# Optimization experiments

Measured on AMD Instinct MI355X. Metric: run time of the kernel, lower is better.

Reference implementation:

```python
import jax, jax.numpy as jnp
import numpy as np

N = 262144   # total sentences
B = 16384    # number of bags
D = 768      # relation_dim
C = 53       # num_classes


def setup_inputs() -> dict:
    key = jax.random.key(0)
    k1, k2, k3, k4 = jax.random.split(key, 4)
    x = jax.random.normal(k1, (N, D), dtype=jnp.float32)
    # xavier_uniform-like init for the relation embedding matrix [C, D]
    limit = float(np.sqrt(6.0 / (C + D)))
    rel_weight = jax.random.uniform(k2, (C, D), dtype=jnp.float32, minval=-limit, maxval=limit)
    bias = jax.random.normal(k3, (C,), dtype=jnp.float32)
    query = jax.random.randint(k4, (N,), 0, C, dtype=jnp.int32)
    # uniform bag boundaries: 0, 16, 32, ..., N  (len B+1)
    input_scope = (jnp.arange(B + 1, dtype=jnp.int32) * (N // B)).astype(jnp.int32)
    return {"x": x, "rel_weight": rel_weight, "bias": bias,
            "input_scope": input_scope, "query": query}


def reference(x, rel_weight, bias, input_scope, query):
    n = x.shape[0]
    num_bags = input_scope.shape[0] - 1
    # segment id of each sentence from bag boundaries (ragged -> segment form)
    seg = jnp.searchsorted(input_scope[1:], jnp.arange(n, dtype=input_scope.dtype), side="right")
    # _train_logits: per-sentence attention score <x_i, rel_emb[query_i]>
    att = jnp.sum(x * rel_weight[query], axis=1)                  # [N]
    # segment-stable softmax within each bag
    m = jax.ops.segment_max(att, seg, num_segments=num_bags)      # [B]
    e = jnp.exp(att - m[seg])                                     # [N]
    z = jax.ops.segment_sum(e, seg, num_segments=num_bags)        # [B]
    w = e / z[seg]                                                # [N]
    # attention-weighted bag representation
    repre = jax.ops.segment_sum(x * w[:, None], seg, num_segments=num_bags)  # [B, D]
    # _logits: bag representation -> class logits
    logits = repre @ rel_weight.T + bias                          # [B, C]
    return logits
```

## Files before the change

kernel.cpp:

```cpp
#include <hip/hip_runtime.h>

#define DIM    768
#define NC     53
#define NCP    64
#define MTB    256
#define NTH    512
#define KSTEP  32
#define NSTEPS 24
#define APAD   40

typedef __attribute__((ext_vector_type(8))) short short8;
typedef __attribute__((ext_vector_type(4))) float f32x4;

static __device__ inline unsigned short f2bf(float f) {
    unsigned u = __float_as_uint(f);
    u += 0x7fff + ((u >> 16) & 1);
    return (unsigned short)(u >> 16);
}

__global__ void wconv_kernel(const float* __restrict__ W, unsigned short* __restrict__ Wt) {
    const int idx = blockIdx.x * 256 + threadIdx.x;
    if (idx >= NCP * DIM) return;
    const int c = idx / DIM, k = idx - c * DIM;
    const float v = (c < NC) ? W[c * DIM + k] : 0.f;
    Wt[idx] = f2bf(v);
}

static __device__ inline void cvt_store(unsigned short* dst, const float4* r) {
    union { short8 v; unsigned short u[8]; } a, b;
    a.u[0]=f2bf(r[0].x); a.u[1]=f2bf(r[0].y); a.u[2]=f2bf(r[0].z); a.u[3]=f2bf(r[0].w);
    a.u[4]=f2bf(r[1].x); a.u[5]=f2bf(r[1].y); a.u[6]=f2bf(r[1].z); a.u[7]=f2bf(r[1].w);
    b.u[0]=f2bf(r[2].x); b.u[1]=f2bf(r[2].y); b.u[2]=f2bf(r[2].z); b.u[3]=f2bf(r[2].w);
    b.u[4]=f2bf(r[3].x); b.u[5]=f2bf(r[3].y); b.u[6]=f2bf(r[3].z); b.u[7]=f2bf(r[3].w);
    *reinterpret_cast<short8*>(dst)     = a.v;
    *reinterpret_cast<short8*>(dst + 8) = b.v;
}

__global__ __launch_bounds__(NTH) void bag_attn_mfma(
    const float* __restrict__ x,
    const unsigned short* __restrict__ Wt,
    const float* __restrict__ bias,
    const int*   __restrict__ query,
    float*       __restrict__ out)
{
    __shared__ __align__(16) unsigned short Ab[2][MTB * APAD];
    __shared__ float att_sm[16][16];
    __shared__ int   qbuf[MTB];

    const int t   = threadIdx.x;
    const int w   = t >> 6;
    const int l   = t & 63;
    const int blk = blockIdx.x;
    const int row_g = blk * MTB;

    if (t < MTB) qbuf[t] = query[row_g + t];

    const int srow  = t >> 1;
    const int shalf = t & 1;
    const float4* x4 = reinterpret_cast<const float4*>(x)
                     + (size_t)(row_g + srow) * (DIM / 4) + shalf * 4;
    unsigned short* dst0 = &Ab[0][srow * APAD + shalf * 16];
    unsigned short* dst1 = &Ab[1][srow * APAD + shalf * 16];

    f32x4 acc[2][4];
    #pragma unroll
    for (int mi = 0; mi < 2; ++mi)
        #pragma unroll
        for (int ni = 0; ni < 4; ++ni)
            acc[mi][ni] = (f32x4){0.f, 0.f, 0.f, 0.f};

    float4 rA[4], rB[4];
    #pragma unroll
    for (int m = 0; m < 4; ++m) rA[m] = x4[0 * 8 + m];
    #pragma unroll
    for (int m = 0; m < 4; ++m) rB[m] = x4[1 * 8 + m];
    cvt_store(dst0, rA);
    __syncthreads();

#define COMPUTE(p, kk)                                                         \
    {                                                                          \
        short8 bfr[4];                                                         \
        _Pragma("unroll")                                                      \
        for (int ni = 0; ni < 4; ++ni)                                         \
            bfr[ni] = *reinterpret_cast<const short8*>(                        \
                Wt + ((16 * ni + (l & 15)) * DIM + (kk) * KSTEP + (l >> 4) * 8)); \
        short8 afr[2];                                                         \
        _Pragma("unroll")                                                      \
        for (int mi = 0; mi < 2; ++mi)                                         \
            afr[mi] = *reinterpret_cast<const short8*>(                        \
                &Ab[p][(32 * w + 16 * mi + (l & 15)) * APAD + (l >> 4) * 8]);  \
        _Pragma("unroll")                                                      \
        for (int mi = 0; mi < 2; ++mi)                                         \
            _Pragma("unroll")                                                  \
            for (int ni = 0; ni < 4; ++ni)                                     \
                acc[mi][ni] = __builtin_amdgcn_mfma_f32_16x16x32_bf16(         \
                    afr[mi], bfr[ni], acc[mi][ni], 0, 0, 0);                   \
    }

    for (int kk = 0; kk < NSTEPS; kk += 2) {
        if (kk + 2 < NSTEPS) {
            #pragma unroll
            for (int m = 0; m < 4; ++m) rA[m] = x4[(kk + 2) * 8 + m];
        }
        COMPUTE(0, kk);
        cvt_store(dst1, rB);
        __syncthreads();
        if (kk + 3 < NSTEPS) {
            #pragma unroll
            for (int m = 0; m < 4; ++m) rB[m] = x4[(kk + 3) * 8 + m];
        }
        COMPUTE(1, kk + 1);
        if (kk + 2 < NSTEPS) {
            cvt_store(dst0, rA);
            __syncthreads();
        }
    }
#undef COMPUTE

    #pragma unroll
    for (int mi = 0; mi < 2; ++mi) {
        #pragma unroll
        for (int r = 0; r < 4; ++r) {
            const int s_loc = ((l >> 4) << 2) + r;
            const int q = qbuf[32 * w + 16 * mi + s_loc];
            if ((q & 15) == (l & 15)) {
                float v = acc[mi][0][r];
                if ((q >> 4) == 1) v = acc[mi][1][r];
                if ((q >> 4) == 2) v = acc[mi][2][r];
                if ((q >> 4) == 3) v = acc[mi][3][r];
                att_sm[2 * w + mi][s_loc] = v;
            }
        }
    }
    __syncthreads();

    #pragma unroll
    for (int mi = 0; mi < 2; ++mi) {
        const int bag = 2 * w + mi;
        const float4* a4 = reinterpret_cast<const float4*>(&att_sm[bag][0]);
        const float4 A0 = a4[0], A1 = a4[1], A2 = a4[2], A3 = a4[3];
        float mx = fmaxf(fmaxf(fmaxf(A0.x, A0.y), fmaxf(A0.z, A0.w)),
                  fmaxf(fmaxf(fmaxf(A1.x, A1.y), fmaxf(A1.z, A1.w)),
                  fmaxf(fmaxf(fmaxf(A2.x, A2.y), fmaxf(A2.z, A2.w)),
                        fmaxf(fmaxf(A3.x, A3.y), fmaxf(A3.z, A3.w)))));
        float zz = __expf(A0.x-mx)+__expf(A0.y-mx)+__expf(A0.z-mx)+__expf(A0.w-mx)
                 + __expf(A1.x-mx)+__expf(A1.y-mx)+__expf(A1.z-mx)+__expf(A1.w-mx)
                 + __expf(A2.x-mx)+__expf(A2.y-mx)+__expf(A2.z-mx)+__expf(A2.w-mx)
                 + __expf(A3.x-mx)+__expf(A3.y-mx)+__expf(A3.z-mx)+__expf(A3.w-mx);
        const float inv = 1.f / zz;
        const int grp = l >> 4;
        float4 As = A0;
        if (grp == 1) As = A1;
        if (grp == 2) As = A2;
        if (grp == 3) As = A3;
        const float w0 = __expf(As.x - mx) * inv;
        const float w1 = __expf(As.y - mx) * inv;
        const float w2 = __expf(As.z - mx) * inv;
        const float w3 = __expf(As.w - mx) * inv;
        #pragma unroll
        for (int ni = 0; ni < 4; ++ni) {
            float p = w0 * acc[mi][ni][0] + w1 * acc[mi][ni][1]
                    + w2 * acc[mi][ni][2] + w3 * acc[mi][ni][3];
            p += __shfl_xor(p, 16, 64);
            p += __shfl_xor(p, 32, 64);
            if (l < 16) {
                const int c = 16 * ni + l;
                if (c < NC)
                    out[(size_t)(blk * 16 + bag) * NC + c] = p + bias[c];
            }
        }
    }
}

extern "C" void kernel_launch(void* const* d_in, const int* in_sizes, int n_in,
                              void* d_out, int out_size, void* d_ws, size_t ws_size,
                              hipStream_t stream) {
    const float* x     = (const float*)d_in[0];
    const float* W     = (const float*)d_in[1];
    const float* bias  = (const float*)d_in[2];
    const int*   query = (const int*)d_in[4];
    float* out = (float*)d_out;

    unsigned short* Wt = (unsigned short*)d_ws;

    const int nrows  = in_sizes[0] / DIM;
    const int nblk   = nrows / MTB;

    wconv_kernel<<<(NCP * DIM + 255) / 256, 256, 0, stream>>>(W, Wt);
    bag_attn_mfma<<<nblk, NTH, 0, stream>>>(x, Wt, bias, query, out);
}
```

Baseline: 202.8 us.

## Load MFMA A-fragments directly from global into registers, dropping LDS staging

Each lane now loads the fp32 x elements it needs for its MFMA A operand straight from global memory and converts them to bf16 in registers. This removes the double-buffered LDS tile, its stores and the per-step __syncthreads barriers. The query prefetch and the barrier after writing att_sm are also dropped, since each wave reads back only the bags it wrote. The change adds an occupancy hint and uses the hardware bf16 pack conversion; in exchange, global loads become narrower per-row segments, which may hurt coalescing.

```diff
diff --git a/kernel.cpp b/kernel.cpp
--- a/kernel.cpp
+++ b/kernel.cpp
@@ -1,13 +1,12 @@
 #include <hip/hip_runtime.h>
+#include <hip/hip_bf16.h>
 
 #define DIM    768
 #define NC     53
 #define NCP    64
 #define MTB    256
 #define NTH    512
-#define KSTEP  32
 #define NSTEPS 24
-#define APAD   40
 
 typedef __attribute__((ext_vector_type(8))) short short8;
 typedef __attribute__((ext_vector_type(4))) float f32x4;
@@ -22,30 +21,26 @@
     const int idx = blockIdx.x * 256 + threadIdx.x;
     if (idx >= NCP * DIM) return;
     const int c = idx / DIM, k = idx - c * DIM;
-    const float v = (c < NC) ? W[c * DIM + k] : 0.f;
-    Wt[idx] = f2bf(v);
+    Wt[idx] = f2bf((c < NC) ? W[c * DIM + k] : 0.f);
 }
 
-static __device__ inline void cvt_store(unsigned short* dst, const float4* r) {
-    union { short8 v; unsigned short u[8]; } a, b;
-    a.u[0]=f2bf(r[0].x); a.u[1]=f2bf(r[0].y); a.u[2]=f2bf(r[0].z); a.u[3]=f2bf(r[0].w);
-    a.u[4]=f2bf(r[1].x); a.u[5]=f2bf(r[1].y); a.u[6]=f2bf(r[1].z); a.u[7]=f2bf(r[1].w);
-    b.u[0]=f2bf(r[2].x); b.u[1]=f2bf(r[2].y); b.u[2]=f2bf(r[2].z); b.u[3]=f2bf(r[2].w);
-    b.u[4]=f2bf(r[3].x); b.u[5]=f2bf(r[3].y); b.u[6]=f2bf(r[3].z); b.u[7]=f2bf(r[3].w);
-    *reinterpret_cast<short8*>(dst)     = a.v;
-    *reinterpret_cast<short8*>(dst + 8) = b.v;
+static __device__ inline short8 cvt8(const float4 a, const float4 b) {
+    union { __hip_bfloat162 h[4]; short8 s; } u;
+    u.h[0] = __float22bfloat162_rn(make_float2(a.x, a.y));
+    u.h[1] = __float22bfloat162_rn(make_float2(a.z, a.w));
+    u.h[2] = __float22bfloat162_rn(make_float2(b.x, b.y));
+    u.h[3] = __float22bfloat162_rn(make_float2(b.z, b.w));
+    return u.s;
 }
 
-__global__ __launch_bounds__(NTH) void bag_attn_mfma(
+__global__ __launch_bounds__(NTH, 4) void bag_attn_mfma2(
     const float* __restrict__ x,
     const unsigned short* __restrict__ Wt,
     const float* __restrict__ bias,
     const int*   __restrict__ query,
     float*       __restrict__ out)
 {
-    __shared__ __align__(16) unsigned short Ab[2][MTB * APAD];
     __shared__ float att_sm[16][16];
-    __shared__ int   qbuf[MTB];
 
     const int t   = threadIdx.x;
     const int w   = t >> 6;
@@ -53,14 +48,13 @@
     const int blk = blockIdx.x;
     const int row_g = blk * MTB;
 
-    if (t < MTB) qbuf[t] = query[row_g + t];
+    const int r16 = l & 15;
+    const int kq  = l >> 4;
 
-    const int srow  = t >> 1;
-    const int shalf = t & 1;
-    const float4* x4 = reinterpret_cast<const float4*>(x)
-                     + (size_t)(row_g + srow) * (DIM / 4) + shalf * 4;
-    unsigned short* dst0 = &Ab[0][srow * APAD + shalf * 16];
-    unsigned short* dst1 = &Ab[1][srow * APAD + shalf * 16];
+    const float4* a0p = reinterpret_cast<const float4*>(x)
+                      + (size_t)(row_g + 32 * w + r16) * (DIM / 4) + kq * 2;
+    const float4* a1p = a0p + 16 * (DIM / 4);
+    const unsigned short* wb = Wt + r16 * DIM + kq * 8;
 
     f32x4 acc[2][4];
     #pragma unroll
@@ -69,61 +63,50 @@
         for (int ni = 0; ni < 4; ++ni)
             acc[mi][ni] = (f32x4){0.f, 0.f, 0.f, 0.f};
 
-    float4 rA[4], rB[4];
+    float4 P0a = a0p[0], P0b = a0p[1], P1a = a1p[0], P1b = a1p[1];
+    float4 Q0a = a0p[8], Q0b = a0p[9], Q1a = a1p[8], Q1b = a1p[9];
+
     #pragma unroll
-    for (int m = 0; m < 4; ++m) rA[m] = x4[0 * 8 + m];
-    #pragma unroll
-    for (int m = 0; m < 4; ++m) rB[m] = x4[1 * 8 + m];
-    cvt_store(dst0, rA);
-    __syncthreads();
-
-#define COMPUTE(p, kk)                                                         \
-    {                                                                          \
-        short8 bfr[4];                                                         \
-        _Pragma("unroll")                                                      \
-        for (int ni = 0; ni < 4; ++ni)                                         \
-            bfr[ni] = *reinterpret_cast<const short8*>(                        \
-                Wt + ((16 * ni + (l & 15)) * DIM + (kk) * KSTEP + (l >> 4) * 8)); \
-        short8 afr[2];                                                         \
-        _Pragma("unroll")                                                      \
-        for (int mi = 0; mi < 2; ++mi)                                         \
-            afr[mi] = *reinterpret_cast<const short8*>(                        \
-                &Ab[p][(32 * w + 16 * mi + (l & 15)) * APAD + (l >> 4) * 8]);  \
-        _Pragma("unroll")                                                      \
-        for (int mi = 0; mi < 2; ++mi)                                         \
-            _Pragma("unroll")                                                  \
-            for (int ni = 0; ni < 4; ++ni)                                     \
-                acc[mi][ni] = __builtin_amdgcn_mfma_f32_16x16x32_bf16(         \
-                    afr[mi], bfr[ni], acc[mi][ni], 0, 0, 0);                   \
-    }
-
     for (int kk = 0; kk < NSTEPS; kk += 2) {
-        if (kk + 2 < NSTEPS) {
+        {
+            const short8 af0 = cvt8(P0a, P0b);
+            const short8 af1 = cvt8(P1a, P1b);
+            if (kk + 2 < NSTEPS) {
+                P0a = a0p[(kk + 2) * 8 + 0]; P0b = a0p[(kk + 2) * 8 + 1];
+                P1a = a1p[(kk + 2) * 8 + 0]; P1b = a1p[(kk + 2) * 8 + 1];
+            }
             #pragma unroll
-            for (int m = 0; m < 4; ++m) rA[m] = x4[(kk + 2) * 8 + m];
+            for (int ni = 0; ni < 4; ++ni) {
+                const short8 bf = *reinterpret_cast<const short8*>(
+                    wb + ni * 16 * DIM + kk * 32);
+                acc[0][ni] = __builtin_amdgcn_mfma_f32_16x16x32_bf16(af0, bf, acc[0][ni], 0, 0, 0);
+                acc[1][ni] = __builtin_amdgcn_mfma_f32_16x16x32_bf16(af1, bf, acc[1][ni], 0, 0, 0);
+            }
         }
-        COMPUTE(0, kk);
-        cvt_store(dst1, rB);
-        __syncthreads();
-        if (kk + 3 < NSTEPS) {
+        {
+            const short8 ag0 = cvt8(Q0a, Q0b);
+            const short8 ag1 = cvt8(Q1a, Q1b);
+            if (kk + 3 < NSTEPS) {
+                Q0a = a0p[(kk + 3) * 8 + 0]; Q0b = a0p[(kk + 3) * 8 + 1];
+                Q1a = a1p[(kk + 3) * 8 + 0]; Q1b = a1p[(kk + 3) * 8 + 1];
+            }
             #pragma unroll
-            for (int m = 0; m < 4; ++m) rB[m] = x4[(kk + 3) * 8 + m];
-        }
-        COMPUTE(1, kk + 1);
-        if (kk + 2 < NSTEPS) {
-            cvt_store(dst0, rA);
-            __syncthreads();
+            for (int ni = 0; ni < 4; ++ni) {
+                const short8 bf = *reinterpret_cast<const short8*>(
+                    wb + ni * 16 * DIM + (kk + 1) * 32);
+                acc[0][ni] = __builtin_amdgcn_mfma_f32_16x16x32_bf16(ag0, bf, acc[0][ni], 0, 0, 0);
+                acc[1][ni] = __builtin_amdgcn_mfma_f32_16x16x32_bf16(ag1, bf, acc[1][ni], 0, 0, 0);
+            }
         }
     }
-#undef COMPUTE
 
     #pragma unroll
     for (int mi = 0; mi < 2; ++mi) {
         #pragma unroll
         for (int r = 0; r < 4; ++r) {
-            const int s_loc = ((l >> 4) << 2) + r;
-            const int q = qbuf[32 * w + 16 * mi + s_loc];
-            if ((q & 15) == (l & 15)) {
+            const int s_loc = (kq << 2) + r;
+            const int q = query[row_g + 32 * w + 16 * mi + s_loc];
+            if ((q & 15) == r16) {
                 float v = acc[mi][0][r];
                 if ((q >> 4) == 1) v = acc[mi][1][r];
                 if ((q >> 4) == 2) v = acc[mi][2][r];
@@ -132,7 +115,6 @@
             }
         }
     }
-    __syncthreads();
 
     #pragma unroll
     for (int mi = 0; mi < 2; ++mi) {
@@ -148,11 +130,10 @@
                  + __expf(A2.x-mx)+__expf(A2.y-mx)+__expf(A2.z-mx)+__expf(A2.w-mx)
                  + __expf(A3.x-mx)+__expf(A3.y-mx)+__expf(A3.z-mx)+__expf(A3.w-mx);
         const float inv = 1.f / zz;
-        const int grp = l >> 4;
         float4 As = A0;
-        if (grp == 1) As = A1;
-        if (grp == 2) As = A2;
-        if (grp == 3) As = A3;
+        if (kq == 1) As = A1;
+        if (kq == 2) As = A2;
+        if (kq == 3) As = A3;
         const float w0 = __expf(As.x - mx) * inv;
         const float w1 = __expf(As.y - mx) * inv;
         const float w2 = __expf(As.z - mx) * inv;
@@ -183,9 +164,9 @@
 
     unsigned short* Wt = (unsigned short*)d_ws;
 
-    const int nrows  = in_sizes[0] / DIM;
-    const int nblk   = nrows / MTB;
+    const int nrows = in_sizes[0] / DIM;
+    const int nblk  = nrows / MTB;
 
     wconv_kernel<<<(NCP * DIM + 255) / 256, 256, 0, stream>>>(W, Wt);
-    bag_attn_mfma<<<nblk, NTH, 0, stream>>>(x, Wt, bias, query, out);
+    bag_attn_mfma2<<<nblk, NTH, 0, stream>>>(x, Wt, bias, query, out);
 }
```

Measured after the change: 212.6 us. +4.8%, slower.
